# Kernel tuning notes

Hardware: AMD Instinct MI355X
Metric: run time of the kernel (lower is better)

The kernel has to match this reference:

```python
import jax, jax.numpy as jnp
import numpy as np

EPS = 1e-6
K_NN = 20
ATTEN_C = 16
NEG_SLOPE = 0.2


def _normalize(v, axis, eps=1e-12):
    n = jnp.linalg.norm(v, axis=axis, keepdims=True)
    return v / jnp.maximum(n, eps)


def channel_equi_vec_normalize(x):
    # x: [B, C, 3, ...]
    x_dir = _normalize(x, axis=2)
    x_norm = jnp.linalg.norm(x, axis=2, keepdims=True)
    return x_dir * _normalize(x_norm, axis=1)


def vn_linear_leaky_relu(x, Wf, Wd, slope=NEG_SLOPE):
    # x: [B, Cin, 3, ...]; Wf, Wd: [Cout, Cin]
    p = jnp.einsum('oi,bi...->bo...', Wf, x)
    d = jnp.einsum('oi,bi...->bo...', Wd, x)
    dot = (p * d).sum(2, keepdims=True)
    d2 = (d * d).sum(2, keepdims=True)
    neg = p - (dot / (d2 + EPS)) * d
    return slope * p + (1.0 - slope) * jnp.where(dot >= 0, p, neg)


def get_graph_feature(y, k):
    # y: [B, 1, 3, N] -> edge features [B, 2, 3, N, K]
    pts = y[:, 0]                                   # [B,3,N]
    xx = (pts ** 2).sum(1)                          # [B,N]
    inner = jnp.einsum('bdn,bdm->bnm', pts, pts)    # [B,N,N]
    neg_dist = 2.0 * inner - xx[:, :, None] - xx[:, None, :]
    _, idx = jax.lax.top_k(neg_dist, k)             # [B,N,K]
    feat = jnp.transpose(y, (0, 3, 1, 2))           # [B,N,C=1,3]
    nbr = jax.vmap(lambda f, i: f[i])(feat, idx)    # [B,N,K,C,3]
    center = jnp.broadcast_to(feat[:, :, None], nbr.shape)
    edge = jnp.concatenate([nbr - center, center], axis=3)  # [B,N,K,2C,3]
    return jnp.transpose(edge, (0, 3, 4, 1, 2))     # [B,2C,3,N,K]


def setup_inputs() -> dict:
    key = jax.random.key(0)
    ks = jax.random.split(key, 6)
    B, N, C = 8, 2048, 64
    return {
        'x': jax.random.normal(ks[0], (B, 3, N), dtype=jnp.float32),
        'y': jax.random.normal(ks[1], (B, 3, N), dtype=jnp.float32),
        'Wf1': jax.random.normal(ks[2], (C, 1), dtype=jnp.float32) * 0.5,
        'Wd1': jax.random.normal(ks[3], (C, 1), dtype=jnp.float32) * 0.5,
        'Wf2': jax.random.normal(ks[4], (C, 2), dtype=jnp.float32) * 0.5,
        'Wd2': jax.random.normal(ks[5], (C, 2), dtype=jnp.float32) * 0.5,
    }


def reference(x, y, Wf1, Wd1, Wf2, Wd2):
    # q branch: [B,1,3,N] -> [B,C,3,N]
    q_x = channel_equi_vec_normalize(vn_linear_leaky_relu(x[:, None], Wf1, Wd1))
    # k/v branch: kNN edge features -> VN-MLP -> [B,C,3,N,K]
    ye = get_graph_feature(y[:, None], K_NN)
    yf = vn_linear_leaky_relu(ye, Wf2, Wd2)
    # per-channel dot between normalized edge features and query
    qk = (channel_equi_vec_normalize(yf) * q_x[..., None]).sum(2)  # [B,C,N,K]
    B, C, N, K = qk.shape
    n_head = C // ATTEN_C
    qk_c = qk.reshape(B, n_head, ATTEN_C, N, K)
    atten = jax.nn.softmax(qk_c.sum(2, keepdims=True) / np.sqrt(3.0 * ATTEN_C), axis=-1)
    atten = jnp.broadcast_to(atten, qk_c.shape).reshape(B, C, N, K)[:, :, None]  # [B,C,1,N,K]
    return (atten * yf).sum(-1)  # [B,C,3,N]
```

## Files before the change

### kernel.cpp

```cpp
#include <hip/hip_runtime.h>
#include <hip/hip_bf16.h>
#include <math.h>

#define BDIM 8
#define NPTS 2048
#define KNN 20
#define NCH 64
#define EPSV 1e-6f

#define SWZ(v, code) __uint_as_float(__builtin_amdgcn_ds_swizzle(__float_as_uint(v), (code)))

__global__ __launch_bounds__(256) void xx_kernel(const float* __restrict__ y,
                                                 float* __restrict__ xx) {
    const int t = blockIdx.x * 256 + threadIdx.x;
    const int b = t >> 11, m = t & (NPTS - 1);
    const float* yb = y + (size_t)b * 3 * NPTS;
    const float a = yb[m], c = yb[NPTS + m], d = yb[2 * NPTS + m];
    xx[t] = a * a + c * c + d * d;
}

__global__ __launch_bounds__(256) void fused_kernel(
    const float* __restrict__ x, const float* __restrict__ y,
    const float* __restrict__ Wf1, const float* __restrict__ Wd1,
    const float* __restrict__ Wf2, const float* __restrict__ Wd2,
    const float* __restrict__ xx, float* __restrict__ out) {
    __shared__ uint2 cand[4][128];
    __shared__ float4 gram[4][KNN][2];
    __shared__ int knn_lds[4][KNN];

    const int wave = threadIdx.x >> 6;
    const int lane = threadIdx.x & 63;
    const int n = blockIdx.x * 4 + wave;
    const int b = blockIdx.y;
    const float* yb = y + (size_t)b * 3 * NPTS;
    const float* xxb = xx + (size_t)b * NPTS;

    const float yn0 = yb[n], yn1 = yb[NPTS + n], yn2 = yb[2 * NPTS + n];
    const float y20 = 2.0f * yn0, y21 = 2.0f * yn1, y22 = 2.0f * yn2;
    const float xxn = yn0 * yn0 + yn1 * yn1 + yn2 * yn2;

    const int c = lane;
    const float x0 = x[((size_t)b * 3 + 0) * NPTS + n];
    const float x1 = x[((size_t)b * 3 + 1) * NPTS + n];
    const float x2 = x[((size_t)b * 3 + 2) * NPTS + n];
    const float xq = x0 * x0 + x1 * x1 + x2 * x2;
    const float f = Wf1[c], g = Wd1[c];
    const float dot1 = f * g * xq;
    const float d21 = g * g * xq;
    const float coef1 = dot1 / (d21 + EPSV);
    const float s_neg = f - coef1 * g;
    const float sxc = 0.2f * f + 0.8f * ((dot1 >= 0.0f) ? f : s_neg);
    const float qn2 = sxc * sxc * xq;
    float totq = qn2;
    totq += SWZ(totq, 0x041F);
    totq += SWZ(totq, 0x081F);
    totq += SWZ(totq, 0x101F);
    totq += SWZ(totq, 0x201F);
    totq += SWZ(totq, 0x401F);
    totq += __shfl_xor(totq, 32);
    const float qn = sqrtf(qn2);
    const float qscale = (1.0f / fmaxf(qn, 1e-12f)) * (qn / fmaxf(sqrtf(totq), 1e-12f));
    const float qs = sxc * qscale;

    const int base_m = lane * 32;
    const float4* r0 = (const float4*)(yb + base_m);
    const float4* r1 = (const float4*)(yb + NPTS + base_m);
    const float4* r2 = (const float4*)(yb + 2 * NPTS + base_m);
    const float4* rx = (const float4*)(xxb + base_m);

    float dist[32];
    float t0 = -INFINITY, t1 = -INFINITY;
#pragma unroll
    for (int q = 0; q < 8; ++q) {
        const float4 a0 = r0[q], a1 = r1[q], a2 = r2[q], ax = rx[q];
#define DCOMP(t, c0, c1, c2, xm)                                          \
        {                                                                  \
            const float d = fmaf(y20, (c0),                                \
                            fmaf(y21, (c1), fmaf(y22, (c2), -(xm))));      \
            dist[q * 4 + t] = d;                                           \
            const float hi = fmaxf(t0, d), lo = fminf(t0, d);              \
            t0 = hi;                                                       \
            t1 = fmaxf(t1, lo);                                            \
        }
        DCOMP(0, a0.x, a1.x, a2.x, ax.x)
        DCOMP(1, a0.y, a1.y, a2.y, ax.y)
        DCOMP(2, a0.z, a1.z, a2.z, ax.z)
        DCOMP(3, a0.w, a1.w, a2.w, ax.w)
#undef DCOMP
    }

    float key = t1;
#pragma unroll
    for (int size = 2; size <= 64; size <<= 1) {
#pragma unroll
        for (int stride = size >> 1; stride > 0; stride >>= 1) {
            const float other = __shfl_xor(key, stride);
            const bool low = (lane & stride) == 0;
            const bool up = (lane & size) == 0;
            key = (low == up) ? fmaxf(key, other) : fminf(key, other);
        }
    }
    const float tau = __shfl(key, 9);

    int wbase = 0;
#pragma unroll
    for (int j = 0; j < 32; ++j) {
        const bool pred = dist[j] >= tau;
        const unsigned long long bal = __ballot(pred);
        const int off = (int)__builtin_amdgcn_mbcnt_hi(
            (unsigned)(bal >> 32),
            __builtin_amdgcn_mbcnt_lo((unsigned)bal, 0u));
        const int slot = wbase + off;
        const int idx = (pred && slot < 64) ? slot : (64 + lane);
        cand[wave][idx] = make_uint2(__float_as_uint(dist[j]),
                                     (unsigned)(base_m + j));
        wbase += (int)__popcll(bal);
    }
    const int C = wbase;

    if (C <= 64) {
        const uint2 e = cand[wave][(lane < C) ? lane : 0];
        const float v = __uint_as_float(e.x);
        const int mm = (int)e.y;
        int rank = 0;
        for (int s = 0; s < C; ++s) {
            const uint2 o = cand[wave][s];
            const float ov = __uint_as_float(o.x);
            rank += (ov > v || (ov == v && (int)o.y < mm)) ? 1 : 0;
        }
        if (lane < C && rank < KNN) knn_lds[wave][rank] = mm;
    } else {
        for (int i = 0; i < KNN; ++i) {
            float bv = dist[0];
            int bj = 0;
#pragma unroll
            for (int j = 1; j < 32; ++j)
                if (dist[j] > bv) { bv = dist[j]; bj = j; }
            int bm = base_m + bj;
            for (int off = 32; off > 0; off >>= 1) {
                const float ov = __shfl_xor(bv, off);
                const int om = __shfl_xor(bm, off);
                if (ov > bv || (ov == bv && om < bm)) { bv = ov; bm = om; }
            }
            if ((bm >> 5) == lane) {
                const int jw = bm & 31;
#pragma unroll
                for (int jj = 0; jj < 32; ++jj)
                    if (jj == jw) dist[jj] = -INFINITY;
            }
            if (lane == 0) knn_lds[wave][i] = bm;
        }
    }

    const float yy = xxn;
    const float yx = yn0 * x0 + yn1 * x1 + yn2 * x2;

    if (lane < KNN) {
        const int mk = knn_lds[wave][lane];
        const float e0 = yb[mk] - yn0;
        const float e1 = yb[NPTS + mk] - yn1;
        const float e2 = yb[2 * NPTS + mk] - yn2;
        gram[wave][lane][0] = make_float4(e0 * e0 + e1 * e1 + e2 * e2,
                                          e0 * yn0 + e1 * yn1 + e2 * yn2,
                                          e0 * x0 + e1 * x1 + e2 * x2, 0.0f);
        gram[wave][lane][1] = make_float4(e0, e1, e2, 0.0f);
    }

    const float wf0 = Wf2[2 * c], wf1v = Wf2[2 * c + 1];
    const float wd0 = Wd2[2 * c], wd1v = Wd2[2 * c + 1];
    const float cA = wf0 * wd0, cB = wf0 * wd1v + wf1v * wd0, cC = wf1v * wd1v;
    const float dA = wd0 * wd0, dB = 2.0f * wd0 * wd1v, dC = wd1v * wd1v;

    float u[KNN], t2[KNN], hh[KNN];
#pragma unroll
    for (int k = 0; k < KNN; ++k) {
        const float4 gv = gram[wave][k][0];
        const float ee = gv.x, ey = gv.y, ex = gv.z;
        const float dt = cA * ee + cB * ey + cC * yy;
        const float dd = dA * ee + dB * ey + dC * yy;
        const float cf = dt * __builtin_amdgcn_rcpf(dd + EPSV);
        const float uu = (dt < 0.0f) ? 0.8f * cf : 0.0f;
        u[k] = uu;
        const float a = wf0 - uu * wd0;
        const float bb = wf1v - uu * wd1v;
        t2[k] = a * (a * ee + bb * ey) + bb * (a * ey + bb * yy);
        hh[k] = qs * (a * ex + bb * yx);
    }

#pragma unroll
    for (int k = 0; k < KNN; ++k) t2[k] += SWZ(t2[k], 0x041F);
#pragma unroll
    for (int k = 0; k < KNN; ++k) t2[k] += SWZ(t2[k], 0x081F);
#pragma unroll
    for (int k = 0; k < KNN; ++k) t2[k] += SWZ(t2[k], 0x101F);
#pragma unroll
    for (int k = 0; k < KNN; ++k) t2[k] += SWZ(t2[k], 0x201F);
#pragma unroll
    for (int k = 0; k < KNN; ++k) t2[k] += SWZ(t2[k], 0x401F);
#pragma unroll
    for (int k = 0; k < KNN; ++k) t2[k] += __shfl_xor(t2[k], 32);
#pragma unroll
    for (int k = 0; k < KNN; ++k) hh[k] += SWZ(hh[k], 0x041F);
#pragma unroll
    for (int k = 0; k < KNN; ++k) hh[k] += SWZ(hh[k], 0x081F);
#pragma unroll
    for (int k = 0; k < KNN; ++k) hh[k] += SWZ(hh[k], 0x101F);
#pragma unroll
    for (int k = 0; k < KNN; ++k) hh[k] += SWZ(hh[k], 0x201F);

    float att[KNN];
    float mx = -INFINITY;
#pragma unroll
    for (int k = 0; k < KNN; ++k) {
        const float rs = __builtin_amdgcn_rsqf(fmaxf(t2[k], 1e-24f));
        att[k] = hh[k] * rs * 0.14433756729740643f;
        mx = fmaxf(mx, att[k]);
    }
    float se = 0.0f;
#pragma unroll
    for (int k = 0; k < KNN; ++k) {
        att[k] = __expf(att[k] - mx);
        se += att[k];
    }
    const float inv = __builtin_amdgcn_rcpf(se);

    float o0 = 0.0f, o1 = 0.0f, o2 = 0.0f, bs = 0.0f;
#pragma unroll
    for (int k = 0; k < KNN; ++k) {
        const float4 ev = gram[wave][k][1];
        const float a = wf0 - u[k] * wd0;
        const float bb = wf1v - u[k] * wd1v;
        const float w = att[k] * inv;
        const float wa = w * a;
        bs += w * bb;
        o0 += wa * ev.x;
        o1 += wa * ev.y;
        o2 += wa * ev.z;
    }

    float* ob = out + (((size_t)b * NCH + c) * 3) * NPTS + n;
    ob[0] = o0 + bs * yn0;
    ob[NPTS] = o1 + bs * yn1;
    ob[2 * NPTS] = o2 + bs * yn2;
}

extern "C" void kernel_launch(void* const* d_in, const int* in_sizes, int n_in,
                              void* d_out, int out_size, void* d_ws, size_t ws_size,
                              hipStream_t stream) {
    const float* x = (const float*)d_in[0];
    const float* y = (const float*)d_in[1];
    const float* Wf1 = (const float*)d_in[2];
    const float* Wd1 = (const float*)d_in[3];
    const float* Wf2 = (const float*)d_in[4];
    const float* Wd2 = (const float*)d_in[5];
    float* out = (float*)d_out;
    float* xx = (float*)d_ws;

    xx_kernel<<<dim3(BDIM * NPTS / 256), 256, 0, stream>>>(y, xx);
    dim3 grid(NPTS / 4, BDIM);
    fused_kernel<<<grid, 256, 0, stream>>>(x, y, Wf1, Wd1, Wf2, Wd2, xx, out);
}
```

Before: 162.5 us.

## Cut registers in fused kNN attention kernel and remap block order

Several independent changes land together: launch bounds now request higher occupancy, block indices are swizzled across the point range, and the candidate buffer shrinks with a sentinel fill so the rank loop can be fully unrolled. The intermediate knn_lds round-trip is removed, so each lane writes its neighbour's gram entry directly. The u and att arrays are dropped by recomputing the gating coefficient in the output loop, and the softmax max-subtraction is removed so exp, sum and output accumulate in one pass. Skipping the max subtraction risks overflow if the scores grow large, though the scaled cosine values here stay small.

```diff
diff --git a/kernel.cpp b/kernel.cpp
--- a/kernel.cpp
+++ b/kernel.cpp
@@ -7,6 +7,7 @@
 #define KNN 20
 #define NCH 64
 #define EPSV 1e-6f
+#define CPAD 64
 
 #define SWZ(v, code) __uint_as_float(__builtin_amdgcn_ds_swizzle(__float_as_uint(v), (code)))
 
@@ -19,18 +20,18 @@
     xx[t] = a * a + c * c + d * d;
 }
 
-__global__ __launch_bounds__(256) void fused_kernel(
+__global__ __launch_bounds__(256, 8) void fused_kernel(
     const float* __restrict__ x, const float* __restrict__ y,
     const float* __restrict__ Wf1, const float* __restrict__ Wd1,
     const float* __restrict__ Wf2, const float* __restrict__ Wd2,
     const float* __restrict__ xx, float* __restrict__ out) {
-    __shared__ uint2 cand[4][128];
+    __shared__ uint2 cand[4][CPAD];
     __shared__ float4 gram[4][KNN][2];
-    __shared__ int knn_lds[4][KNN];
 
     const int wave = threadIdx.x >> 6;
     const int lane = threadIdx.x & 63;
-    const int n = blockIdx.x * 4 + wave;
+    const int g = (blockIdx.x & 7) * 64 + (blockIdx.x >> 3);
+    const int n = g * 4 + wave;
     const int b = blockIdx.y;
     const float* yb = y + (size_t)b * 3 * NPTS;
     const float* xxb = xx + (size_t)b * NPTS;
@@ -44,11 +45,11 @@
     const float x1 = x[((size_t)b * 3 + 1) * NPTS + n];
     const float x2 = x[((size_t)b * 3 + 2) * NPTS + n];
     const float xq = x0 * x0 + x1 * x1 + x2 * x2;
-    const float f = Wf1[c], g = Wd1[c];
-    const float dot1 = f * g * xq;
-    const float d21 = g * g * xq;
-    const float coef1 = dot1 / (d21 + EPSV);
-    const float s_neg = f - coef1 * g;
+    const float f = Wf1[c], gg = Wd1[c];
+    const float dot1 = f * gg * xq;
+    const float d21 = gg * gg * xq;
+    const float coef1 = dot1 * __builtin_amdgcn_rcpf(d21 + EPSV);
+    const float s_neg = f - coef1 * gg;
     const float sxc = 0.2f * f + 0.8f * ((dot1 >= 0.0f) ? f : s_neg);
     const float qn2 = sxc * sxc * xq;
     float totq = qn2;
@@ -62,6 +63,8 @@
     const float qscale = (1.0f / fmaxf(qn, 1e-12f)) * (qn / fmaxf(sqrtf(totq), 1e-12f));
     const float qs = sxc * qscale;
 
+    cand[wave][lane] = make_uint2(0xFF800000u , 0x7fffffffu);
+
     const int base_m = lane * 32;
     const float4* r0 = (const float4*)(yb + base_m);
     const float4* r1 = (const float4*)(yb + NPTS + base_m);
@@ -69,27 +72,36 @@
     const float4* rx = (const float4*)(xxb + base_m);
 
     float dist[32];
-    float t0 = -INFINITY, t1 = -INFINITY;
+    float t0a = -INFINITY, t1a = -INFINITY;
+    float t0b = -INFINITY, t1b = -INFINITY;
 #pragma unroll
     for (int q = 0; q < 8; ++q) {
         const float4 a0 = r0[q], a1 = r1[q], a2 = r2[q], ax = rx[q];
-#define DCOMP(t, c0, c1, c2, xm)                                          \
+#define DCOMP(t, c0, c1, c2, xm, T0, T1)                                   \
         {                                                                  \
             const float d = fmaf(y20, (c0),                                \
                             fmaf(y21, (c1), fmaf(y22, (c2), -(xm))));      \
             dist[q * 4 + t] = d;                                           \
-            const float hi = fmaxf(t0, d), lo = fminf(t0, d);              \
-            t0 = hi;                                                       \
-            t1 = fmaxf(t1, lo);                                            \
-        }
-        DCOMP(0, a0.x, a1.x, a2.x, ax.x)
-        DCOMP(1, a0.y, a1.y, a2.y, ax.y)
-        DCOMP(2, a0.z, a1.z, a2.z, ax.z)
-        DCOMP(3, a0.w, a1.w, a2.w, ax.w)
+            const float hi = fmaxf(T0, d), lo = fminf(T0, d);              \
+            T0 = hi;                                                       \
+            T1 = fmaxf(T1, lo);                                            \
+        }
+        if (q < 4) {
+            DCOMP(0, a0.x, a1.x, a2.x, ax.x, t0a, t1a)
+            DCOMP(1, a0.y, a1.y, a2.y, ax.y, t0a, t1a)
+            DCOMP(2, a0.z, a1.z, a2.z, ax.z, t0a, t1a)
+            DCOMP(3, a0.w, a1.w, a2.w, ax.w, t0a, t1a)
+        } else {
+            DCOMP(0, a0.x, a1.x, a2.x, ax.x, t0b, t1b)
+            DCOMP(1, a0.y, a1.y, a2.y, ax.y, t0b, t1b)
+            DCOMP(2, a0.z, a1.z, a2.z, ax.z, t0b, t1b)
+            DCOMP(3, a0.w, a1.w, a2.w, ax.w, t0b, t1b)
+        }
 #undef DCOMP
     }
-
-    float key = t1;
+    const float t1m = fmaxf(fminf(t0a, t0b), fmaxf(t1a, t1b));
+
+    float key = t1m;
 #pragma unroll
     for (int size = 2; size <= 64; size <<= 1) {
 #pragma unroll
@@ -111,25 +123,29 @@
             (unsigned)(bal >> 32),
             __builtin_amdgcn_mbcnt_lo((unsigned)bal, 0u));
         const int slot = wbase + off;
-        const int idx = (pred && slot < 64) ? slot : (64 + lane);
-        cand[wave][idx] = make_uint2(__float_as_uint(dist[j]),
-                                     (unsigned)(base_m + j));
+        if (pred && slot < CPAD)
+            cand[wave][slot] = make_uint2(__float_as_uint(dist[j]),
+                                          (unsigned)(base_m + j));
         wbase += (int)__popcll(bal);
     }
     const int C = wbase;
 
-    if (C <= 64) {
-        const uint2 e = cand[wave][(lane < C) ? lane : 0];
+    int myrank = KNN, mym = 0;
+    if (C <= CPAD) {
+        const uint2 e = cand[wave][lane];
         const float v = __uint_as_float(e.x);
         const int mm = (int)e.y;
         int rank = 0;
-        for (int s = 0; s < C; ++s) {
+#pragma unroll
+        for (int s = 0; s < CPAD; ++s) {
             const uint2 o = cand[wave][s];
             const float ov = __uint_as_float(o.x);
             rank += (ov > v || (ov == v && (int)o.y < mm)) ? 1 : 0;
         }
-        if (lane < C && rank < KNN) knn_lds[wave][rank] = mm;
+        myrank = rank;
+        mym = mm;
     } else {
+        int my_sel = 0;
         for (int i = 0; i < KNN; ++i) {
             float bv = dist[0];
             int bj = 0;
@@ -148,30 +164,31 @@
                 for (int jj = 0; jj < 32; ++jj)
                     if (jj == jw) dist[jj] = -INFINITY;
             }
-            if (lane == 0) knn_lds[wave][i] = bm;
-        }
+            if (lane == i) my_sel = bm;
+        }
+        myrank = lane;
+        mym = my_sel;
+    }
+
+    if (myrank < KNN) {
+        const float e0 = yb[mym] - yn0;
+        const float e1 = yb[NPTS + mym] - yn1;
+        const float e2 = yb[2 * NPTS + mym] - yn2;
+        gram[wave][myrank][0] = make_float4(e0 * e0 + e1 * e1 + e2 * e2,
+                                            e0 * yn0 + e1 * yn1 + e2 * yn2,
+                                            e0 * x0 + e1 * x1 + e2 * x2, 0.0f);
+        gram[wave][myrank][1] = make_float4(e0, e1, e2, 0.0f);
     }
 
     const float yy = xxn;
     const float yx = yn0 * x0 + yn1 * x1 + yn2 * x2;
-
-    if (lane < KNN) {
-        const int mk = knn_lds[wave][lane];
-        const float e0 = yb[mk] - yn0;
-        const float e1 = yb[NPTS + mk] - yn1;
-        const float e2 = yb[2 * NPTS + mk] - yn2;
-        gram[wave][lane][0] = make_float4(e0 * e0 + e1 * e1 + e2 * e2,
-                                          e0 * yn0 + e1 * yn1 + e2 * yn2,
-                                          e0 * x0 + e1 * x1 + e2 * x2, 0.0f);
-        gram[wave][lane][1] = make_float4(e0, e1, e2, 0.0f);
-    }
 
     const float wf0 = Wf2[2 * c], wf1v = Wf2[2 * c + 1];
     const float wd0 = Wd2[2 * c], wd1v = Wd2[2 * c + 1];
     const float cA = wf0 * wd0, cB = wf0 * wd1v + wf1v * wd0, cC = wf1v * wd1v;
     const float dA = wd0 * wd0, dB = 2.0f * wd0 * wd1v, dC = wd1v * wd1v;
 
-    float u[KNN], t2[KNN], hh[KNN];
+    float t2[KNN], hh[KNN];
 #pragma unroll
     for (int k = 0; k < KNN; ++k) {
         const float4 gv = gram[wave][k][0];
@@ -180,7 +197,6 @@
         const float dd = dA * ee + dB * ey + dC * yy;
         const float cf = dt * __builtin_amdgcn_rcpf(dd + EPSV);
         const float uu = (dt < 0.0f) ? 0.8f * cf : 0.0f;
-        u[k] = uu;
         const float a = wf0 - uu * wd0;
         const float bb = wf1v - uu * wd1v;
         t2[k] = a * (a * ee + bb * ey) + bb * (a * ey + bb * yy);
@@ -208,40 +224,34 @@
 #pragma unroll
     for (int k = 0; k < KNN; ++k) hh[k] += SWZ(hh[k], 0x201F);
 
-    float att[KNN];
-    float mx = -INFINITY;
+    float lsum = 0.0f, o0 = 0.0f, o1 = 0.0f, o2 = 0.0f, bs = 0.0f;
 #pragma unroll
     for (int k = 0; k < KNN; ++k) {
+        const float4 gv = gram[wave][k][0];
+        const float4 ev = gram[wave][k][1];
         const float rs = __builtin_amdgcn_rsqf(fmaxf(t2[k], 1e-24f));
-        att[k] = hh[k] * rs * 0.14433756729740643f;
-        mx = fmaxf(mx, att[k]);
-    }
-    float se = 0.0f;
-#pragma unroll
-    for (int k = 0; k < KNN; ++k) {
-        att[k] = __expf(att[k] - mx);
-        se += att[k];
-    }
-    const float inv = __builtin_amdgcn_rcpf(se);
-
-    float o0 = 0.0f, o1 = 0.0f, o2 = 0.0f, bs = 0.0f;
-#pragma unroll
-    for (int k = 0; k < KNN; ++k) {
-        const float4 ev = gram[wave][k][1];
-        const float a = wf0 - u[k] * wd0;
-        const float bb = wf1v - u[k] * wd1v;
-        const float w = att[k] * inv;
-        const float wa = w * a;
-        bs += w * bb;
-        o0 += wa * ev.x;
-        o1 += wa * ev.y;
-        o2 += wa * ev.z;
-    }
+        const float s = hh[k] * rs * 0.14433756729740643f;
+        const float p = __expf(s);
+        const float ee = gv.x, ey = gv.y;
+        const float dt = cA * ee + cB * ey + cC * yy;
+        const float dd = dA * ee + dB * ey + dC * yy;
+        const float cf = dt * __builtin_amdgcn_rcpf(dd + EPSV);
+        const float uu = (dt < 0.0f) ? 0.8f * cf : 0.0f;
+        const float a = wf0 - uu * wd0;
+        const float bb = wf1v - uu * wd1v;
+        const float pa = p * a;
+        lsum += p;
+        bs += p * bb;
+        o0 += pa * ev.x;
+        o1 += pa * ev.y;
+        o2 += pa * ev.z;
+    }
+    const float inv = __builtin_amdgcn_rcpf(lsum);
 
     float* ob = out + (((size_t)b * NCH + c) * 3) * NPTS + n;
-    ob[0] = o0 + bs * yn0;
-    ob[NPTS] = o1 + bs * yn1;
-    ob[2 * NPTS] = o2 + bs * yn2;
+    ob[0] = (o0 + bs * yn0) * inv;
+    ob[NPTS] = (o1 + bs * yn1) * inv;
+    ob[2 * NPTS] = (o2 + bs * yn2) * inv;
 }
 
 extern "C" void kernel_launch(void* const* d_in, const int* in_sizes, int n_in,
```

Result: slower. 182.2 us (+12.1%).
